# Performance work log

Hardware: AMD Instinct MI355X
Metric: run time of the kernel (lower is better)

Reference implementation:

```python
import jax, jax.numpy as jnp
import numpy as np

N_PER = 128   # nodes per graph
G = 256       # graphs in batch
DEG = 4       # out-degree per node
IN = 768
H = 256
R = 4         # num_relations
C = 4         # num classes
RATIO = 0.25
N = G * N_PER
E_G = N_PER * DEG
E = G * E_G
K = int(np.ceil(RATIO * E_G))  # edges kept per graph by sparse_topk


def _build_edges():
    # per graph: edges (i, (i+o) mod n) for o in 1..DEG; offsets < n/2 so the
    # symmetrized edge set has no duplicate pairs (torch.unique is a no-op)
    i = np.arange(N_PER)
    src_l = np.concatenate([i for _ in range(DEG)])
    dst_l = np.concatenate([(i + o) % N_PER for o in range(1, DEG + 1)])
    offs = np.repeat(np.arange(G) * N_PER, E_G)
    src = np.tile(src_l, G) + offs
    dst = np.tile(dst_l, G) + offs
    return jnp.asarray(np.stack([src, dst]), dtype=jnp.int32)


def setup_inputs() -> dict:
    key = jax.random.key(0)
    ks = jax.random.split(key, 20)
    s = 0.02
    inp = {
        'x': jax.random.normal(ks[0], (N, IN), jnp.float32),
        'edge_index': _build_edges(),
        'edge_type': jax.random.randint(ks[1], (E,), 0, R, jnp.int32),
        'y': jax.random.randint(ks[2], (G,), 0, C, jnp.int32),
        # Generator
        'gen_w': jax.random.normal(ks[3], (IN, H), jnp.float32) * s,
        'gen_b': jnp.zeros((H,), jnp.float32),
        'att_w1': jax.random.normal(ks[4], (2 * H, 4 * H), jnp.float32) * s,
        'att_b1': jnp.zeros((4 * H,), jnp.float32),
        'att_w2': jax.random.normal(ks[5], (4 * H, 1), jnp.float32) * s,
        'att_b2': jnp.zeros((1,), jnp.float32),
        # RGCNEncoder
        'in_w': jax.random.normal(ks[6], (IN, H), jnp.float32) * s,
        'in_b': jnp.zeros((H,), jnp.float32),
        'rel_w': jax.random.normal(ks[7], (2, R, H, H), jnp.float32) * s,
        'root_w': jax.random.normal(ks[8], (2, H, H), jnp.float32) * s,
        'conv_b': jnp.zeros((2, H), jnp.float32),
        # classifier head
        'cls_w1': jax.random.normal(ks[9], (2 * H, H), jnp.float32) * s,
        'cls_b1': jnp.zeros((H,), jnp.float32),
        'cls_w2': jax.random.normal(ks[10], (H, C), jnp.float32) * s,
        'cls_b2': jnp.zeros((C,), jnp.float32),
    }
    return inp


def _rgcn_encode(x, ei, et, in_w, in_b, rel_w, root_w, conv_b):
    # linear_in + LeakyReLU
    h = jax.nn.leaky_relu(x @ in_w + in_b)
    src, dst = ei[0], ei[1]
    for l in range(2):  # two RGCNConv layers (dropout is identity in eval)
        out = h @ root_w[l] + conv_b[l]
        for r in range(R):  # per-relation gather-transform-scatter, mean aggr
            m = (et == r)
            xw = h @ rel_w[l, r]                            # [N,H]
            msg = jnp.where(m[:, None], xw[src], 0.0)       # [E,H]
            agg = jax.ops.segment_sum(msg, dst, num_segments=N)
            deg = jax.ops.segment_sum(m.astype(h.dtype), dst, num_segments=N)
            out = out + agg / jnp.maximum(deg, 1.0)[:, None]
        h = out
    ptr = jnp.arange(G) * N_PER  # data.ptr[:-1]: first node of each graph
    return h[ptr]                # [G,H]


def reference(x, edge_index, edge_type, y, gen_w, gen_b, att_w1, att_b1,
              att_w2, att_b2, in_w, in_b, rel_w, root_w, conv_b,
              cls_w1, cls_b1, cls_w2, cls_b2):
    src, dst = edge_index[0], edge_index[1]

    # ----- initial representation on the full graph -----
    initial_rep = _rgcn_encode(x, edge_index, edge_type,
                               in_w, in_b, rel_w, root_w, conv_b)

    # ----- Generator: edge scores -----
    hg = jax.nn.leaky_relu(x @ gen_w + gen_b)
    edge_rep = jnp.concatenate([hg[src], hg[dst]], axis=-1)      # [E,2H]
    score = (jax.nn.relu(edge_rep @ att_w1 + att_b1) @ att_w2 + att_b2)
    score = score.reshape(-1)                                    # [E]

    # ----- split_graph: per-graph top-k (ratio=0.25, descending) -----
    # edges are grouped contiguously per graph with E_G edges each
    sg = score.reshape(G, E_G)
    _, idx = jax.lax.top_k(sg, K)                                # [G,K]
    kept = (idx + (jnp.arange(G) * E_G)[:, None]).reshape(-1)    # global ids

    # ----- graph_sample: keep + symmetrize (unique is a no-op here) -----
    ks_, kd_, kt_ = src[kept], dst[kept], edge_type[kept]
    ei2 = jnp.stack([jnp.concatenate([ks_, kd_]),
                     jnp.concatenate([kd_, ks_])])               # [2, 2*G*K]
    et2 = jnp.concatenate([kt_, kt_])

    learned_rep = _rgcn_encode(x, ei2, et2,
                               in_w, in_b, rel_w, root_w, conv_b)

    # ----- classifier + cross entropy -----
    rep = jnp.concatenate([initial_rep, learned_rep], axis=-1)   # [G,2H]
    logits = jax.nn.leaky_relu(rep @ cls_w1 + cls_b1) @ cls_w2 + cls_b2
    logp = jax.nn.log_softmax(logits, axis=-1)
    loss = -jnp.mean(logp[jnp.arange(G), y])
    return (logits, loss, y)
```

## Files before the change

### kernel.cpp

```cpp
#include <hip/hip_runtime.h>
#include <hip/hip_bf16.h>

typedef __bf16 bf16_t;
typedef __bf16 bf16x8 __attribute__((ext_vector_type(8)));
typedef __bf16 bf16x4 __attribute__((ext_vector_type(4)));
typedef float  f32x4  __attribute__((ext_vector_type(4)));

#define NNODES 32768
#define NPER   128
#define NGRAPH 256
#define NEDGE  131072
#define EPERG  512
#define KKEEP  128
#define M1     5376
#define PLANE1 (M1 * 256)

__global__ void prep_kernel(const float* __restrict__ in_w,
                            const float* __restrict__ gen_w,
                            const float* __restrict__ att_w1,
                            const float* __restrict__ rel_w,
                            const float* __restrict__ root_w,
                            const float* __restrict__ in_b,
                            const float* __restrict__ gen_b,
                            bf16_t* __restrict__ wbf,
                            bf16_t* __restrict__ attT,
                            bf16_t* __restrict__ lw,
                            float*  __restrict__ biasws)
{
  int idx = blockIdx.x * 256 + threadIdx.x;
  if (idx < 393216) {
    int which = idx / 196608, rem = idx % 196608;
    int n = rem / 768, k = rem % 768;
    const float* w = which ? gen_w : in_w;
    wbf[idx] = (bf16_t)w[k * 256 + n];
  } else if (idx < 917504) {
    int i2 = idx - 393216;
    int half = i2 / 262144, rem = i2 % 262144;
    int n = rem / 256, k = rem % 256;
    attT[i2] = (bf16_t)att_w1[(half * 256 + k) * 1024 + n];
  } else if (idx < 1572864) {
    int i3 = idx - 917504;
    int l = i3 / 327680, rem = i3 % 327680;
    int z = rem / 65536, r2 = rem % 65536;
    int n = r2 / 256, k = r2 % 256;
    float v = (z == 0) ? root_w[(l * 256 + k) * 256 + n]
                       : rel_w[((l * 4 + (z - 1)) * 256 + k) * 256 + n];
    lw[i3] = (bf16_t)v;
  } else if (idx < 1573376) {
    int j = idx - 1572864;
    biasws[j] = (j < 256) ? in_b[j] : gen_b[j - 256];
  }
}

__global__ void cast_x_kernel(const float* __restrict__ x, bf16_t* __restrict__ xb)
{
  long i = (long)blockIdx.x * 256 + threadIdx.x;
  const float4* xf = (const float4*)x;
  float4 a = xf[i * 2], b = xf[i * 2 + 1];
  bf16x8 v;
  v[0] = (bf16_t)a.x; v[1] = (bf16_t)a.y; v[2] = (bf16_t)a.z; v[3] = (bf16_t)a.w;
  v[4] = (bf16_t)b.x; v[5] = (bf16_t)b.y; v[6] = (bf16_t)b.z; v[7] = (bf16_t)b.w;
  ((bf16x8*)xb)[i] = v;
}

template<int ACT, bool HAS_BIAS, typename OUT_T>
__global__ __launch_bounds__(256, 2) void gemm_bt(
    const bf16_t* __restrict__ A, const bf16_t* __restrict__ BTall,
    const float* __restrict__ biasall, OUT_T* __restrict__ Call,
    int M, int N, int K, long sBz, long sCz)
{
  const bf16_t* BT = BTall + (long)blockIdx.z * sBz;
  OUT_T* C = Call + (long)blockIdx.z * sCz;
  __shared__ bf16_t sA[8192];
  __shared__ bf16_t sB[8192];
  const int tid = threadIdx.x;
  const int lane = tid & 63, wid = tid >> 6;
  const int wr = wid >> 1, wc = wid & 1;
  const long row0 = (long)blockIdx.x * 128;
  const long n0  = (long)blockIdx.y * 128;

  f32x4 acc[4][4];
  #pragma unroll
  for (int m = 0; m < 4; ++m)
    #pragma unroll
    for (int n = 0; n < 4; ++n)
      #pragma unroll
      for (int j = 0; j < 4; ++j) acc[m][n][j] = 0.f;

  for (int kt = 0; kt < K; kt += 64) {
    #pragma unroll
    for (int it = 0; it < 4; ++it) {
      const int P = it * 4096 + tid * 16;
      const int row = P >> 7;
      const int cch = ((P >> 4) & 7) ^ (row & 7);
      const long koff = kt + cch * 8;
      const bf16_t* ga = A  + (row0 + row) * (long)K + koff;
      const bf16_t* gb = BT + (n0  + row) * (long)K + koff;
      bf16_t* la = sA + it * 2048 + wid * 512;
      bf16_t* lb = sB + it * 2048 + wid * 512;
      __builtin_amdgcn_global_load_lds((__attribute__((address_space(1))) void*)ga,
                                       (__attribute__((address_space(3))) void*)la, 16, 0, 0);
      __builtin_amdgcn_global_load_lds((__attribute__((address_space(1))) void*)gb,
                                       (__attribute__((address_space(3))) void*)lb, 16, 0, 0);
    }
    __syncthreads();
    const char* cA = (const char*)sA;
    const char* cB = (const char*)sB;
    #pragma unroll
    for (int kk = 0; kk < 2; ++kk) {
      bf16x8 af[4], bfr[4];
      #pragma unroll
      for (int m = 0; m < 4; ++m) {
        const int row = wr * 64 + m * 16 + (lane & 15);
        const int inb = (((lane >> 4) * 16) + kk * 64) ^ ((row & 7) << 4);
        af[m] = *(const bf16x8*)(cA + row * 128 + inb);
      }
      #pragma unroll
      for (int n = 0; n < 4; ++n) {
        const int row = wc * 64 + n * 16 + (lane & 15);
        const int inb = (((lane >> 4) * 16) + kk * 64) ^ ((row & 7) << 4);
        bfr[n] = *(const bf16x8*)(cB + row * 128 + inb);
      }
      #pragma unroll
      for (int m = 0; m < 4; ++m)
        #pragma unroll
        for (int n = 0; n < 4; ++n)
          acc[m][n] = __builtin_amdgcn_mfma_f32_16x16x32_bf16(af[m], bfr[n], acc[m][n], 0, 0, 0);
    }
    __syncthreads();
  }
  #pragma unroll
  for (int n = 0; n < 4; ++n) {
    const int col = (int)n0 + wc * 64 + n * 16 + (lane & 15);
    float bv = 0.f;
    if (HAS_BIAS) bv = biasall[(long)blockIdx.z * N + col];
    #pragma unroll
    for (int m = 0; m < 4; ++m) {
      #pragma unroll
      for (int j = 0; j < 4; ++j) {
        const long row = row0 + wr * 64 + m * 16 + (lane >> 4) * 4 + j;
        float v = acc[m][n][j] + bv;
        if (ACT == 1) v = (v > 0.f) ? v : 0.01f * v;
        C[row * N + col] = (OUT_T)v;
      }
    }
  }
}

__global__ void score_kernel(const bf16_t* __restrict__ Abuf, const bf16_t* __restrict__ Bbuf,
                             const int* __restrict__ src, const int* __restrict__ dst,
                             const float* __restrict__ b1, const float* __restrict__ w2,
                             const float* __restrict__ b2, float* __restrict__ scores,
                             int edge0, int node0, int nEdges)
{
  __shared__ float sb1[1024], sw2[1024];
  for (int i = threadIdx.x; i < 1024; i += 256) { sb1[i] = b1[i]; sw2[i] = w2[i]; }
  __syncthreads();
  const int wid = threadIdx.x >> 6, lane = threadIdx.x & 63;
  const int e = blockIdx.x * 4 + wid;
  if (e >= nEdges) return;
  const int ge = edge0 + e;
  const int s = src[ge] - node0, d = dst[ge] - node0;
  const bf16x8* ar = (const bf16x8*)(Abuf + (long)s * 1024);
  const bf16x8* br = (const bf16x8*)(Bbuf + (long)d * 1024);
  float acc = 0.f;
  #pragma unroll
  for (int half = 0; half < 2; ++half) {
    bf16x8 av = ar[lane * 2 + half];
    bf16x8 bv = br[lane * 2 + half];
    const int jb = (lane * 2 + half) * 8;
    #pragma unroll
    for (int j = 0; j < 8; ++j) {
      float v = (float)av[j] + (float)bv[j] + sb1[jb + j];
      v = v > 0.f ? v : 0.f;
      acc += v * sw2[jb + j];
    }
  }
  #pragma unroll
  for (int off = 32; off > 0; off >>= 1) acc += __shfl_down(acc, off);
  if (lane == 0) scores[ge] = acc + b2[0];
}

__global__ void topk_kernel(const float* __restrict__ scores,
                            const int* __restrict__ src, const int* __restrict__ dst,
                            const int* __restrict__ et,
                            int* __restrict__ ksrc, int* __restrict__ kdst, int* __restrict__ ktyp)
{
  const int g = blockIdx.x;
  __shared__ float sc[512];
  __shared__ int   id[512];
  for (int i = threadIdx.x; i < 512; i += 256) { sc[i] = scores[g * 512 + i]; id[i] = i; }
  for (int k2 = 2; k2 <= 512; k2 <<= 1) {
    for (int j = k2 >> 1; j > 0; j >>= 1) {
      __syncthreads();
      for (int t = threadIdx.x; t < 512; t += 256) {
        const int p = t ^ j;
        if (p > t) {
          float s1 = sc[t], s2 = sc[p];
          int   i1 = id[t], i2 = id[p];
          bool kgt = (s1 < s2) || (s1 == s2 && i1 > i2);
          bool up  = ((t & k2) == 0);
          if (kgt == up) { sc[t] = s2; sc[p] = s1; id[t] = i2; id[p] = i1; }
        }
      }
    }
  }
  __syncthreads();
  if (threadIdx.x < 128) {
    const int e = g * 512 + id[threadIdx.x];
    const int o = g * 128 + threadIdx.x;
    ksrc[o] = src[e]; kdst[o] = dst[e]; ktyp[o] = et[e];
  }
}

__global__ void csr_count(const int* __restrict__ ksrc, const int* __restrict__ kdst,
                          int* __restrict__ counts)
{
  const int i = blockIdx.x * 256 + threadIdx.x;
  if (i >= NGRAPH * KKEEP) return;
  atomicAdd(&counts[kdst[i]], 1);
  atomicAdd(&counts[ksrc[i]], 1);
}

__global__ void csr_offsets(const int* __restrict__ counts, int* __restrict__ offs,
                            int* __restrict__ cursor)
{
  const int g = blockIdx.x, t = threadIdx.x;
  __shared__ int s[128];
  const int mc = counts[g * 128 + t];
  s[t] = mc;
  __syncthreads();
  for (int dd = 1; dd < 128; dd <<= 1) {
    int v = (t >= dd) ? s[t - dd] : 0;
    __syncthreads();
    s[t] += v;
    __syncthreads();
  }
  const int o = g * 256 + (s[t] - mc);
  offs[g * 128 + t] = o;
  cursor[g * 128 + t] = o;
}

__global__ void csr_fill(const int* __restrict__ ksrc, const int* __restrict__ kdst,
                         const int* __restrict__ ktyp, int* __restrict__ cursor,
                         int* __restrict__ nsrc, int* __restrict__ ntyp)
{
  const int i = blockIdx.x * 256 + threadIdx.x;
  if (i >= NGRAPH * KKEEP) return;
  const int s = ksrc[i], d = kdst[i], t = ktyp[i];
  int p = atomicAdd(&cursor[d], 1); nsrc[p] = s; ntyp[p] = t;
  int q = atomicAdd(&cursor[s], 1); nsrc[q] = d; ntyp[q] = t;
}


__global__ void agg_struct_sel(const bf16_t* __restrict__ xw0, const int* __restrict__ et,
                               const float* __restrict__ conv_b, bf16_t* __restrict__ h1g)
{
  const int wid = threadIdx.x >> 6, lane = threadIdx.x & 63;
  const int row = blockIdx.x * 4 + wid;
  const int g = row / 5, slot = row % 5;
  const int d = (slot == 0) ? 0 : (128 - slot);
  const int n = g * 128 + d;
  const int c = lane * 4;
  int rt[4], si[4];
  #pragma unroll
  for (int oo = 0; oo < 4; ++oo) {
    const int i = (d - oo - 1 + 128) & 127;
    rt[oo] = et[g * 512 + oo * 128 + i];
    si[oo] = g * 128 + i;
  }
  const float4 cb = *(const float4*)(conv_b + c);
  bf16x4 rv = *(const bf16x4*)(xw0 + (long)n * 256 + c);
  float acc[4] = { (float)rv[0] + cb.x, (float)rv[1] + cb.y,
                   (float)rv[2] + cb.z, (float)rv[3] + cb.w };
  float s0[4] = {0,0,0,0}, s1[4] = {0,0,0,0}, s2[4] = {0,0,0,0}, s3[4] = {0,0,0,0};
  int d0 = 0, d1 = 0, d2 = 0, d3 = 0;
  #pragma unroll
  for (int oo = 0; oo < 4; ++oo) {
    const int t = rt[oo];
    bf16x4 w = *(const bf16x4*)(xw0 + ((long)(t + 1) * NNODES + si[oo]) * 256 + c);
    if (t == 0)      { d0++; for (int j = 0; j < 4; ++j) s0[j] += (float)w[j]; }
    else if (t == 1) { d1++; for (int j = 0; j < 4; ++j) s1[j] += (float)w[j]; }
    else if (t == 2) { d2++; for (int j = 0; j < 4; ++j) s2[j] += (float)w[j]; }
    else             { d3++; for (int j = 0; j < 4; ++j) s3[j] += (float)w[j]; }
  }
  if (d0) { float r = 1.f / d0; for (int j = 0; j < 4; ++j) acc[j] += s0[j] * r; }
  if (d1) { float r = 1.f / d1; for (int j = 0; j < 4; ++j) acc[j] += s1[j] * r; }
  if (d2) { float r = 1.f / d2; for (int j = 0; j < 4; ++j) acc[j] += s2[j] * r; }
  if (d3) { float r = 1.f / d3; for (int j = 0; j < 4; ++j) acc[j] += s3[j] * r; }
  bf16x4 ov; for (int j = 0; j < 4; ++j) ov[j] = (bf16_t)acc[j];
  *(bf16x4*)(h1g + (long)row * 256 + c) = ov;
}

__global__ void agg_csr_sel(const bf16_t* __restrict__ xw0, const int* __restrict__ offs,
                            const int* __restrict__ cnts, const int* __restrict__ nsrc,
                            const int* __restrict__ ntyp, const float* __restrict__ conv_b,
                            bf16_t* __restrict__ h1g)
{
  const int wid = threadIdx.x >> 6, lane = threadIdx.x & 63;
  const int idx = blockIdx.x * 4 + wid;
  const int g = idx >> 4, slot = idx & 15;
  const int off0 = offs[g * 128], cnt0 = cnts[g * 128];
  if (slot > cnt0) return;
  const int v = (slot == 0) ? g * 128 : nsrc[off0 + slot - 1];
  const int row = 1280 + idx;
  const int offv = offs[v], cntv = cnts[v];
  const int c = lane * 4;
  const float4 cb = *(const float4*)(conv_b + c);
  bf16x4 rv = *(const bf16x4*)(xw0 + (long)v * 256 + c);
  float acc[4] = { (float)rv[0] + cb.x, (float)rv[1] + cb.y,
                   (float)rv[2] + cb.z, (float)rv[3] + cb.w };
  float s0[4] = {0,0,0,0}, s1[4] = {0,0,0,0}, s2[4] = {0,0,0,0}, s3[4] = {0,0,0,0};
  int d0 = 0, d1 = 0, d2 = 0, d3 = 0;
  for (int j = 0; j < cntv; ++j) {
    const int t = ntyp[offv + j];
    const int sv = nsrc[offv + j];
    bf16x4 w = *(const bf16x4*)(xw0 + ((long)(t + 1) * NNODES + sv) * 256 + c);
    if (t == 0)      { d0++; for (int q = 0; q < 4; ++q) s0[q] += (float)w[q]; }
    else if (t == 1) { d1++; for (int q = 0; q < 4; ++q) s1[q] += (float)w[q]; }
    else if (t == 2) { d2++; for (int q = 0; q < 4; ++q) s2[q] += (float)w[q]; }
    else             { d3++; for (int q = 0; q < 4; ++q) s3[q] += (float)w[q]; }
  }
  if (d0) { float r = 1.f / d0; for (int q = 0; q < 4; ++q) acc[q] += s0[q] * r; }
  if (d1) { float r = 1.f / d1; for (int q = 0; q < 4; ++q) acc[q] += s1[q] * r; }
  if (d2) { float r = 1.f / d2; for (int q = 0; q < 4; ++q) acc[q] += s2[q] * r; }
  if (d3) { float r = 1.f / d3; for (int q = 0; q < 4; ++q) acc[q] += s3[q] * r; }
  bf16x4 ov; for (int q = 0; q < 4; ++q) ov[q] = (bf16_t)acc[q];
  *(bf16x4*)(h1g + (long)row * 256 + c) = ov;
}

__global__ void fagg_init(const bf16_t* __restrict__ xw1, const int* __restrict__ et,
                          const float* __restrict__ conv_b1, float* __restrict__ h2I)
{
  const int wid = threadIdx.x >> 6, lane = threadIdx.x & 63;
  const int g = blockIdx.x * 4 + wid;
  const int base = g * 5;
  const int c = lane * 4;
  const float4 cb = *(const float4*)(conv_b1 + c);
  bf16x4 rv = *(const bf16x4*)(xw1 + (long)base * 256 + c);
  float acc[4] = { (float)rv[0] + cb.x, (float)rv[1] + cb.y,
                   (float)rv[2] + cb.z, (float)rv[3] + cb.w };
  float s0[4] = {0,0,0,0}, s1[4] = {0,0,0,0}, s2[4] = {0,0,0,0}, s3[4] = {0,0,0,0};
  int d0 = 0, d1 = 0, d2 = 0, d3 = 0;
  #pragma unroll
  for (int o = 1; o <= 4; ++o) {
    const int t = et[g * 512 + (o - 1) * 128 + (128 - o)];
    bf16x4 w = *(const bf16x4*)(xw1 + ((long)(t + 1) * M1 + base + o) * 256 + c);
    if (t == 0)      { d0++; for (int q = 0; q < 4; ++q) s0[q] += (float)w[q]; }
    else if (t == 1) { d1++; for (int q = 0; q < 4; ++q) s1[q] += (float)w[q]; }
    else if (t == 2) { d2++; for (int q = 0; q < 4; ++q) s2[q] += (float)w[q]; }
    else             { d3++; for (int q = 0; q < 4; ++q) s3[q] += (float)w[q]; }
  }
  if (d0) { float r = 1.f / d0; for (int q = 0; q < 4; ++q) acc[q] += s0[q] * r; }
  if (d1) { float r = 1.f / d1; for (int q = 0; q < 4; ++q) acc[q] += s1[q] * r; }
  if (d2) { float r = 1.f / d2; for (int q = 0; q < 4; ++q) acc[q] += s2[q] * r; }
  if (d3) { float r = 1.f / d3; for (int q = 0; q < 4; ++q) acc[q] += s3[q] * r; }
  *(float4*)(h2I + (long)g * 256 + c) = make_float4(acc[0], acc[1], acc[2], acc[3]);
}

__global__ void fagg_learn(const bf16_t* __restrict__ xw1, const int* __restrict__ offs,
                           const int* __restrict__ cnts, const int* __restrict__ ntyp,
                           const float* __restrict__ conv_b1, float* __restrict__ h2L)
{
  const int wid = threadIdx.x >> 6, lane = threadIdx.x & 63;
  const int g = blockIdx.x * 4 + wid;
  const int base = 1280 + g * 16;
  const int off0 = offs[g * 128], cnt0 = cnts[g * 128];
  const int c = lane * 4;
  const float4 cb = *(const float4*)(conv_b1 + c);
  bf16x4 rv = *(const bf16x4*)(xw1 + (long)base * 256 + c);
  float acc[4] = { (float)rv[0] + cb.x, (float)rv[1] + cb.y,
                   (float)rv[2] + cb.z, (float)rv[3] + cb.w };
  float s0[4] = {0,0,0,0}, s1[4] = {0,0,0,0}, s2[4] = {0,0,0,0}, s3[4] = {0,0,0,0};
  int d0 = 0, d1 = 0, d2 = 0, d3 = 0;
  for (int j = 0; j < cnt0; ++j) {
    const int t = ntyp[off0 + j];
    bf16x4 w = *(const bf16x4*)(xw1 + ((long)(t + 1) * M1 + base + 1 + j) * 256 + c);
    if (t == 0)      { d0++; for (int q = 0; q < 4; ++q) s0[q] += (float)w[q]; }
    else if (t == 1) { d1++; for (int q = 0; q < 4; ++q) s1[q] += (float)w[q]; }
    else if (t == 2) { d2++; for (int q = 0; q < 4; ++q) s2[q] += (float)w[q]; }
    else             { d3++; for (int q = 0; q < 4; ++q) s3[q] += (float)w[q]; }
  }
  if (d0) { float r = 1.f / d0; for (int q = 0; q < 4; ++q) acc[q] += s0[q] * r; }
  if (d1) { float r = 1.f / d1; for (int q = 0; q < 4; ++q) acc[q] += s1[q] * r; }
  if (d2) { float r = 1.f / d2; for (int q = 0; q < 4; ++q) acc[q] += s2[q] * r; }
  if (d3) { float r = 1.f / d3; for (int q = 0; q < 4; ++q) acc[q] += s3[q] * r; }
  *(float4*)(h2L + (long)g * 256 + c) = make_float4(acc[0], acc[1], acc[2], acc[3]);
}

__global__ void classifier_kernel(const float* __restrict__ h2I, const float* __restrict__ h2L,
                                  const float* __restrict__ w1, const float* __restrict__ b1,
                                  const float* __restrict__ w2, const float* __restrict__ b2,
                                  const int* __restrict__ y, float* __restrict__ out,
                                  float* __restrict__ logp)
{
  const int g = blockIdx.x, t = threadIdx.x;
  __shared__ float rep[512];
  __shared__ float hid[256];
  __shared__ float lg[4];
  rep[t] = h2I[g * 256 + t];
  rep[256 + t] = h2L[g * 256 + t];
  __syncthreads();
  float a = b1[t];
  for (int i = 0; i < 512; ++i) a += rep[i] * w1[i * 256 + t];
  hid[t] = a > 0.f ? a : 0.01f * a;
  __syncthreads();
  if (t < 4) {
    float s = b2[t];
    for (int j = 0; j < 256; ++j) s += hid[j] * w2[j * 4 + t];
    lg[t] = s;
    out[g * 4 + t] = s;
  }
  __syncthreads();
  if (t == 0) {
    float m = fmaxf(fmaxf(lg[0], lg[1]), fmaxf(lg[2], lg[3]));
    float se = expf(lg[0] - m) + expf(lg[1] - m) + expf(lg[2] - m) + expf(lg[3] - m);
    logp[g] = lg[y[g]] - (m + logf(se));
  }
}

__global__ void finalize_kernel(const float* __restrict__ logp, const int* __restrict__ y,
                                float* __restrict__ out)
{
  __shared__ float s[256];
  const int t = threadIdx.x;
  s[t] = logp[t];
  __syncthreads();
  for (int d = 128; d > 0; d >>= 1) {
    if (t < d) s[t] += s[t + d];
    __syncthreads();
  }
  if (t == 0) out[1024] = -s[0] / 256.f;
  out[1025 + t] = (float)y[t];
}

extern "C" void kernel_launch(void* const* d_in, const int* in_sizes, int n_in,
                              void* d_out, int out_size, void* d_ws, size_t ws_size,
                              hipStream_t stream)
{
  (void)in_sizes; (void)n_in; (void)out_size; (void)ws_size;
  const float* x      = (const float*)d_in[0];
  const int*   ei     = (const int*)d_in[1];
  const int*   et     = (const int*)d_in[2];
  const int*   y      = (const int*)d_in[3];
  const float* gen_w  = (const float*)d_in[4];
  const float* gen_b  = (const float*)d_in[5];
  const float* att_w1 = (const float*)d_in[6];
  const float* att_b1 = (const float*)d_in[7];
  const float* att_w2 = (const float*)d_in[8];
  const float* att_b2 = (const float*)d_in[9];
  const float* in_w   = (const float*)d_in[10];
  const float* in_b   = (const float*)d_in[11];
  const float* rel_w  = (const float*)d_in[12];
  const float* root_w = (const float*)d_in[13];
  const float* conv_b = (const float*)d_in[14];
  const float* cls_w1 = (const float*)d_in[15];
  const float* cls_b1 = (const float*)d_in[16];
  const float* cls_w2 = (const float*)d_in[17];
  const float* cls_b2 = (const float*)d_in[18];
  const int* src = ei;
  const int* dst = ei + NEDGE;

  char* ws = (char*)d_ws;
  size_t off = 83886080;
  const size_t oBIG = 0;
  auto alloc = [&](size_t bytes) { size_t r = off; off += (bytes + 255) & ~(size_t)255; return r; };
  const size_t oH0  = alloc((size_t)NNODES * 256 * 2);
  const size_t oHG  = alloc((size_t)NNODES * 256 * 2);
  const size_t oH1G = alloc((size_t)M1 * 256 * 2);
  const size_t oXW1 = alloc((size_t)5 * M1 * 256 * 2);
  const size_t oSC  = alloc((size_t)NEDGE * 4);
  const size_t oKS  = alloc((size_t)NGRAPH * KKEEP * 4);
  const size_t oKD  = alloc((size_t)NGRAPH * KKEEP * 4);
  const size_t oKT  = alloc((size_t)NGRAPH * KKEEP * 4);
  const size_t oCNT = alloc((size_t)NNODES * 4);
  const size_t oOFF = alloc((size_t)NNODES * 4);
  const size_t oCUR = alloc((size_t)NNODES * 4);
  const size_t oNS  = alloc((size_t)2 * NGRAPH * KKEEP * 4);
  const size_t oNT  = alloc((size_t)2 * NGRAPH * KKEEP * 4);
  const size_t oWBF = alloc((size_t)2 * 256 * 768 * 2);
  const size_t oATT = alloc((size_t)2 * 1024 * 256 * 2);
  const size_t oLW  = alloc((size_t)2 * 5 * 256 * 256 * 2);
  const size_t oBIA = alloc(512 * 4);
  const size_t oH2I = alloc((size_t)NGRAPH * 256 * 4);
  const size_t oH2L = alloc((size_t)NGRAPH * 256 * 4);
  const size_t oLP  = alloc((size_t)NGRAPH * 4);

  bf16_t* xbf  = (bf16_t*)(ws + oBIG);
  bf16_t* AB   = (bf16_t*)(ws + oBIG);
  bf16_t* xw0  = (bf16_t*)(ws + oBIG);
  bf16_t* h0   = (bf16_t*)(ws + oH0);
  bf16_t* hg   = (bf16_t*)(ws + oHG);
  bf16_t* h1g  = (bf16_t*)(ws + oH1G);
  bf16_t* xw1  = (bf16_t*)(ws + oXW1);
  bf16_t* wbf  = (bf16_t*)(ws + oWBF);
  bf16_t* attT = (bf16_t*)(ws + oATT);
  bf16_t* lw   = (bf16_t*)(ws + oLW);
  float*  bias = (float*)(ws + oBIA);

  prep_kernel<<<6146, 256, 0, stream>>>(in_w, gen_w, att_w1, rel_w, root_w, in_b, gen_b,
                                        wbf, attT, lw, bias);
  cast_x_kernel<<<12288, 256, 0, stream>>>(x, xbf);

  gemm_bt<1, true, bf16_t><<<dim3(256, 2, 2), 256, 0, stream>>>(
      xbf, wbf, bias, h0, NNODES, 256, 768, 196608L, 8388608L);

  for (int c = 0; c < 2; ++c) {
    gemm_bt<0, false, bf16_t><<<dim3(128, 8, 2), 256, 0, stream>>>(
        hg + (long)c * 16384 * 256, attT, nullptr, AB, 16384, 1024, 256, 262144L, 16777216L);
    score_kernel<<<16384, 256, 0, stream>>>(AB, AB + 16777216, src, dst, att_b1, att_w2,
                                            att_b2, (float*)(ws + oSC), c * 65536, c * 16384, 65536);
  }

  topk_kernel<<<NGRAPH, 256, 0, stream>>>((const float*)(ws + oSC), src, dst, et,
                                          (int*)(ws + oKS), (int*)(ws + oKD), (int*)(ws + oKT));
  hipMemsetAsync(ws + oCNT, 0, (size_t)NNODES * 4, stream);
  csr_count<<<128, 256, 0, stream>>>((const int*)(ws + oKS), (const int*)(ws + oKD), (int*)(ws + oCNT));
  csr_offsets<<<NGRAPH, 128, 0, stream>>>((const int*)(ws + oCNT), (int*)(ws + oOFF), (int*)(ws + oCUR));
  csr_fill<<<128, 256, 0, stream>>>((const int*)(ws + oKS), (const int*)(ws + oKD),
                                    (const int*)(ws + oKT), (int*)(ws + oCUR),
                                    (int*)(ws + oNS), (int*)(ws + oNT));

  gemm_bt<0, false, bf16_t><<<dim3(256, 2, 5), 256, 0, stream>>>(
      h0, lw, nullptr, xw0, NNODES, 256, 256, 65536L, 8388608L);

  agg_struct_sel<<<320, 256, 0, stream>>>(xw0, et, conv_b, h1g);
  agg_csr_sel<<<1024, 256, 0, stream>>>(xw0, (const int*)(ws + oOFF), (const int*)(ws + oCNT),
                                        (const int*)(ws + oNS), (const int*)(ws + oNT),
                                        conv_b, h1g);

  gemm_bt<0, false, bf16_t><<<dim3(42, 2, 5), 256, 0, stream>>>(
      h1g, lw + 5 * 65536, nullptr, xw1, M1, 256, 256, 65536L, (long)PLANE1);

  fagg_init<<<64, 256, 0, stream>>>(xw1, et, conv_b + 256, (float*)(ws + oH2I));
  fagg_learn<<<64, 256, 0, stream>>>(xw1, (const int*)(ws + oOFF), (const int*)(ws + oCNT),
                                     (const int*)(ws + oNT), conv_b + 256, (float*)(ws + oH2L));

  classifier_kernel<<<NGRAPH, 256, 0, stream>>>((const float*)(ws + oH2I), (const float*)(ws + oH2L),
                                                cls_w1, cls_b1, cls_w2, cls_b2, y,
                                                (float*)d_out, (float*)(ws + oLP));
  finalize_kernel<<<1, 256, 0, stream>>>((const float*)(ws + oLP), y, (float*)d_out);
}
```

Measured before the change: 489.9 us.

## Widen GEMM tiles to 128x256 with 512 threads and merge attention chunks

The batched GEMM kernel now runs 512-thread blocks computing 128x256 output tiles. The z-batched weight planes are treated as one concatenated N dimension, and output columns are remapped into per-slab planes. This halves how often each A tile is reloaded and cuts launch count. The two-chunk attention GEMM plus score loop becomes one full-size pass, which needs a larger workspace. The bigger tiles lower occupancy to one block per CU and use more LDS.

```diff
diff --git a/kernel.cpp b/kernel.cpp
--- a/kernel.cpp
+++ b/kernel.cpp
@@ -64,20 +64,18 @@
 }
 
 template<int ACT, bool HAS_BIAS, typename OUT_T>
-__global__ __launch_bounds__(256, 2) void gemm_bt(
-    const bf16_t* __restrict__ A, const bf16_t* __restrict__ BTall,
-    const float* __restrict__ biasall, OUT_T* __restrict__ Call,
-    int M, int N, int K, long sBz, long sCz)
-{
-  const bf16_t* BT = BTall + (long)blockIdx.z * sBz;
-  OUT_T* C = Call + (long)blockIdx.z * sCz;
+__global__ __launch_bounds__(512, 1) void gemm_bt2(
+    const bf16_t* __restrict__ A, const bf16_t* __restrict__ BT,
+    const float* __restrict__ bias, OUT_T* __restrict__ C,
+    int M, int K, int colShift, long slabStride)
+{
   __shared__ bf16_t sA[8192];
-  __shared__ bf16_t sB[8192];
+  __shared__ bf16_t sB[16384];
   const int tid = threadIdx.x;
   const int lane = tid & 63, wid = tid >> 6;
-  const int wr = wid >> 1, wc = wid & 1;
+  const int wr = wid >> 2, wc = wid & 3;
   const long row0 = (long)blockIdx.x * 128;
-  const long n0  = (long)blockIdx.y * 128;
+  const long n0  = (long)blockIdx.y * 256;
 
   f32x4 acc[4][4];
   #pragma unroll
@@ -89,17 +87,22 @@
 
   for (int kt = 0; kt < K; kt += 64) {
     #pragma unroll
-    for (int it = 0; it < 4; ++it) {
-      const int P = it * 4096 + tid * 16;
+    for (int p = 0; p < 2; ++p) {
+      const int P = p * 8192 + tid * 16;
       const int row = P >> 7;
       const int cch = ((P >> 4) & 7) ^ (row & 7);
-      const long koff = kt + cch * 8;
-      const bf16_t* ga = A  + (row0 + row) * (long)K + koff;
-      const bf16_t* gb = BT + (n0  + row) * (long)K + koff;
-      bf16_t* la = sA + it * 2048 + wid * 512;
-      bf16_t* lb = sB + it * 2048 + wid * 512;
+      const bf16_t* ga = A + (row0 + row) * (long)K + kt + cch * 8;
+      bf16_t* la = sA + p * 4096 + wid * 512;
       __builtin_amdgcn_global_load_lds((__attribute__((address_space(1))) void*)ga,
                                        (__attribute__((address_space(3))) void*)la, 16, 0, 0);
+    }
+    #pragma unroll
+    for (int q = 0; q < 4; ++q) {
+      const int P = q * 8192 + tid * 16;
+      const int row = P >> 7;
+      const int cch = ((P >> 4) & 7) ^ (row & 7);
+      const bf16_t* gb = BT + (n0 + row) * (long)K + kt + cch * 8;
+      bf16_t* lb = sB + q * 4096 + wid * 512;
       __builtin_amdgcn_global_load_lds((__attribute__((address_space(1))) void*)gb,
                                        (__attribute__((address_space(3))) void*)lb, 16, 0, 0);
     }
@@ -129,11 +132,14 @@
     }
     __syncthreads();
   }
+  const int ncolsM1 = (1 << colShift) - 1;
   #pragma unroll
   for (int n = 0; n < 4; ++n) {
     const int col = (int)n0 + wc * 64 + n * 16 + (lane & 15);
+    const int slab = col >> colShift;
+    const int cin = col & ncolsM1;
     float bv = 0.f;
-    if (HAS_BIAS) bv = biasall[(long)blockIdx.z * N + col];
+    if (HAS_BIAS) bv = bias[col];
     #pragma unroll
     for (int m = 0; m < 4; ++m) {
       #pragma unroll
@@ -141,7 +147,7 @@
         const long row = row0 + wr * 64 + m * 16 + (lane >> 4) * 4 + j;
         float v = acc[m][n][j] + bv;
         if (ACT == 1) v = (v > 0.f) ? v : 0.01f * v;
-        C[row * N + col] = (OUT_T)v;
+        C[(long)slab * slabStride + (row << colShift) + cin] = (OUT_T)v;
       }
     }
   }
@@ -150,17 +156,14 @@
 __global__ void score_kernel(const bf16_t* __restrict__ Abuf, const bf16_t* __restrict__ Bbuf,
                              const int* __restrict__ src, const int* __restrict__ dst,
                              const float* __restrict__ b1, const float* __restrict__ w2,
-                             const float* __restrict__ b2, float* __restrict__ scores,
-                             int edge0, int node0, int nEdges)
+                             const float* __restrict__ b2, float* __restrict__ scores)
 {
   __shared__ float sb1[1024], sw2[1024];
   for (int i = threadIdx.x; i < 1024; i += 256) { sb1[i] = b1[i]; sw2[i] = w2[i]; }
   __syncthreads();
   const int wid = threadIdx.x >> 6, lane = threadIdx.x & 63;
   const int e = blockIdx.x * 4 + wid;
-  if (e >= nEdges) return;
-  const int ge = edge0 + e;
-  const int s = src[ge] - node0, d = dst[ge] - node0;
+  const int s = src[e], d = dst[e];
   const bf16x8* ar = (const bf16x8*)(Abuf + (long)s * 1024);
   const bf16x8* br = (const bf16x8*)(Bbuf + (long)d * 1024);
   float acc = 0.f;
@@ -178,7 +181,7 @@
   }
   #pragma unroll
   for (int off = 32; off > 0; off >>= 1) acc += __shfl_down(acc, off);
-  if (lane == 0) scores[ge] = acc + b2[0];
+  if (lane == 0) scores[e] = acc + b2[0];
 }
 
 __global__ void topk_kernel(const float* __restrict__ scores,
@@ -462,7 +465,7 @@
   const int* dst = ei + NEDGE;
 
   char* ws = (char*)d_ws;
-  size_t off = 83886080;
+  size_t off = 134217728;
   const size_t oBIG = 0;
   auto alloc = [&](size_t bytes) { size_t r = off; off += (bytes + 255) & ~(size_t)255; return r; };
   const size_t oH0  = alloc((size_t)NNODES * 256 * 2);
@@ -502,15 +505,13 @@
                                         wbf, attT, lw, bias);
   cast_x_kernel<<<12288, 256, 0, stream>>>(x, xbf);
 
-  gemm_bt<1, true, bf16_t><<<dim3(256, 2, 2), 256, 0, stream>>>(
-      xbf, wbf, bias, h0, NNODES, 256, 768, 196608L, 8388608L);
-
-  for (int c = 0; c < 2; ++c) {
-    gemm_bt<0, false, bf16_t><<<dim3(128, 8, 2), 256, 0, stream>>>(
-        hg + (long)c * 16384 * 256, attT, nullptr, AB, 16384, 1024, 256, 262144L, 16777216L);
-    score_kernel<<<16384, 256, 0, stream>>>(AB, AB + 16777216, src, dst, att_b1, att_w2,
-                                            att_b2, (float*)(ws + oSC), c * 65536, c * 16384, 65536);
-  }
+  gemm_bt2<1, true, bf16_t><<<dim3(256, 2), 512, 0, stream>>>(
+      xbf, wbf, bias, h0, NNODES, 768, 8, 8388608L);
+
+  gemm_bt2<0, false, bf16_t><<<dim3(256, 8), 512, 0, stream>>>(
+      hg, attT, nullptr, AB, NNODES, 256, 10, 33554432L);
+  score_kernel<<<32768, 256, 0, stream>>>(AB, AB + 33554432L, src, dst, att_b1, att_w2,
+                                          att_b2, (float*)(ws + oSC));
 
   topk_kernel<<<NGRAPH, 256, 0, stream>>>((const float*)(ws + oSC), src, dst, et,
                                           (int*)(ws + oKS), (int*)(ws + oKD), (int*)(ws + oKT));
@@ -521,16 +522,16 @@
                                     (const int*)(ws + oKT), (int*)(ws + oCUR),
                                     (int*)(ws + oNS), (int*)(ws + oNT));
 
-  gemm_bt<0, false, bf16_t><<<dim3(256, 2, 5), 256, 0, stream>>>(
-      h0, lw, nullptr, xw0, NNODES, 256, 256, 65536L, 8388608L);
+  gemm_bt2<0, false, bf16_t><<<dim3(256, 5), 512, 0, stream>>>(
+      h0, lw, nullptr, xw0, NNODES, 256, 8, 8388608L);
 
   agg_struct_sel<<<320, 256, 0, stream>>>(xw0, et, conv_b, h1g);
   agg_csr_sel<<<1024, 256, 0, stream>>>(xw0, (const int*)(ws + oOFF), (const int*)(ws + oCNT),
                                         (const int*)(ws + oNS), (const int*)(ws + oNT),
                                         conv_b, h1g);
 
-  gemm_bt<0, false, bf16_t><<<dim3(42, 2, 5), 256, 0, stream>>>(
-      h1g, lw + 5 * 65536, nullptr, xw1, M1, 256, 256, 65536L, (long)PLANE1);
+  gemm_bt2<0, false, bf16_t><<<dim3(42, 5), 512, 0, stream>>>(
+      h1g, lw + 5 * 65536, nullptr, xw1, M1, 256, 8, (long)PLANE1);
 
   fagg_init<<<64, 256, 0, stream>>>(xw1, et, conv_b + 256, (float*)(ws + oH2I));
   fagg_learn<<<64, 256, 0, stream>>>(xw1, (const int*)(ws + oOFF), (const int*)(ws + oCNT),
```

New measurement: 494.4 us. Within noise of the previous version (+0.9%).
